# Kernel optimization log

Measured on AMD Instinct MI355X. Metric: run time of the kernel, lower is better.

## Reference

```python
import jax, jax.numpy as jnp
import numpy as np

N_HEADS = 8
D_MODEL = 256
HEAD_DEPTH = D_MODEL // N_HEADS
B, S = 2, 4096


def setup_inputs() -> dict:
    key = jax.random.key(0)
    ks = jax.random.split(key, 8)
    scale = 1.0 / np.sqrt(D_MODEL)
    return {
        "q": jax.random.normal(ks[0], (B, S, D_MODEL), dtype=jnp.float32),
        "k": jax.random.normal(ks[1], (B, S, D_MODEL), dtype=jnp.float32),
        "v": jax.random.normal(ks[2], (B, S, D_MODEL), dtype=jnp.float32),
        "mask": jax.random.randint(ks[3], (B, S, S), 0, 2).astype(jnp.bool_),
        "wq": jax.random.normal(ks[4], (D_MODEL, D_MODEL), dtype=jnp.float32) * scale,
        "wk": jax.random.normal(ks[5], (D_MODEL, D_MODEL), dtype=jnp.float32) * scale,
        "wv": jax.random.normal(ks[6], (D_MODEL, D_MODEL), dtype=jnp.float32) * scale,
        "w_out": jax.random.normal(ks[7], (D_MODEL, D_MODEL), dtype=jnp.float32) * scale,
    }


def _split_heads(x):
    # [B, S, D] -> [B, H, S, Dh]
    b, s, _ = x.shape
    return x.reshape(b, s, N_HEADS, HEAD_DEPTH).transpose(0, 2, 1, 3)


def reference(q, k, v, mask, wq, wk, wv, w_out):
    Q = _split_heads(q @ wq)
    K = _split_heads(k @ wk)
    V = _split_heads(v @ wv)
    # [B, H, Sq, Sk]
    scores = jnp.einsum('bhqd,bhkd->bhqk', Q, K) / jnp.sqrt(
        jnp.asarray(HEAD_DEPTH, dtype=Q.dtype))
    # mask True -> -inf, broadcast over heads
    scores = jnp.where(mask[:, None, :, :], -jnp.inf, scores)
    probs = jax.nn.softmax(scores, axis=-1)
    attn = jnp.einsum('bhqk,bhkd->bhqd', probs, V)
    attn = attn.transpose(0, 2, 1, 3).reshape(q.shape[0], -1, D_MODEL)
    return attn @ w_out
```

## Files before the change

### kernel.cpp

```cpp
#include <hip/hip_runtime.h>
#include <stdint.h>

typedef __bf16 bf16;
typedef __bf16 bf16x2 __attribute__((ext_vector_type(2)));
typedef __bf16 bf16x4 __attribute__((ext_vector_type(4)));
typedef __bf16 bf16x8 __attribute__((ext_vector_type(8)));
typedef float  f32x4  __attribute__((ext_vector_type(4)));
typedef float  f32x16 __attribute__((ext_vector_type(16)));
typedef float  float4v __attribute__((ext_vector_type(4)));
typedef int    int4v   __attribute__((ext_vector_type(4)));
typedef unsigned int uint;
typedef uint   uint4v  __attribute__((ext_vector_type(4)));
typedef unsigned long long ull;

#define QSCALE 0.25505003984214403f


__global__ __launch_bounds__(256) void transpose_w(
    const float* __restrict__ w0, const float* __restrict__ w1,
    const float* __restrict__ w2, const float* __restrict__ w3,
    bf16* __restrict__ WT) {
  const int wsel = blockIdx.z;
  const float* W = wsel == 0 ? w0 : wsel == 1 ? w1 : wsel == 2 ? w2 : w3;
  const int k0 = blockIdx.x * 64, n0 = blockIdx.y * 64;
  __shared__ __align__(16) bf16 t[64][72];
  const int tid = threadIdx.x;
  {
    const int kk = (tid >> 4) << 2;
    const int nn = (tid & 15) << 2;
#pragma unroll
    for (int r = 0; r < 4; ++r) {
      float4v a = *(const float4v*)(W + (size_t)(k0 + kk + r) * 256 + n0 + nn);
#pragma unroll
      for (int j = 0; j < 4; ++j) t[nn + j][kk + r] = (bf16)a[j];
    }
  }
  __syncthreads();
  {
    const int ni = tid >> 2;
    const int c  = (tid & 3) * 16;
    bf16x8 o0 = *(const bf16x8*)(&t[ni][c]);
    bf16x8 o1 = *(const bf16x8*)(&t[ni][c + 8]);
    bf16* dst = WT + (size_t)wsel * 65536 + (size_t)(n0 + ni) * 256 + k0 + c;
    *(bf16x8*)dst = o0;
    *(bf16x8*)(dst + 8) = o1;
  }
}

__global__ __launch_bounds__(256) void proj_pack(
    const float* __restrict__ xq, const float* __restrict__ xk, const float* __restrict__ xv,
    const bf16* __restrict__ WT,
    bf16* __restrict__ Qp, bf16* __restrict__ Kp, bf16* __restrict__ Vp,
    const int* __restrict__ mask, uint* __restrict__ M2) {
  __shared__ __align__(16) unsigned char smem[18432];
  const int tid = threadIdx.x;

  if (blockIdx.x < 1024) {
    uint* trans = (uint*)smem;
    const int pid = blockIdx.x;
    const int bb = pid >> 9;
    const int qt = (pid >> 2) & 127;
    const int kc = pid & 3;
    const int q0 = qt * 32;
    const int w = tid >> 6, l = tid & 63;
    const int d2 = l & 7;
    const int sh = 8 * d2;
    for (int batch = 0; batch < 4; ++batch) {
      int4v m[8];
#pragma unroll
      for (int u = 0; u < 8; ++u) {
        const int q_l = w * 8 + batch * 2 + (u >> 2);
        const int c = u & 3;
        m[u] = *(const int4v*)(mask + ((size_t)(bb * 4096 + q0 + q_l)) * 4096 +
                               kc * 1024 + c * 256 + 4 * l);
      }
#pragma unroll
      for (int u = 0; u < 8; ++u) {
        const int q_l = w * 8 + batch * 2 + (u >> 2);
        const int c = u & 3;
        uint out = 0;
#pragma unroll
        for (int i = 0; i < 4; ++i) {
          ull b = __ballot(m[u][i] != 0);
          out |= ((uint)(b >> sh) & 0xFFu) << (8 * i);
        }
        if (l < 8) trans[(c * 8 + d2) * 36 + q_l] = out;
      }
    }
    __syncthreads();
    {
      const int r = tid >> 3, c4 = (tid & 7) * 4;
      int4v a = *(const int4v*)(trans + r * 36 + c4);
      *(int4v*)(M2 + ((size_t)(bb * 128 + kc * 32 + r)) * 4096 + q0 + c4) = a;
    }
    return;
  }

  const int pb = blockIdx.x - 1024;
  const int z = pb >> 8;
  const int r8 = pb & 255;
  const int m0 = (r8 >> 1) * 64, n0 = (r8 & 1) * 128;
  const float* X = z == 0 ? xq : (z == 1 ? xk : xv);
  const bf16* wt = WT + (size_t)z * 65536;
  const int wave = tid >> 6, lane = tid & 63;
  const int nl = lane & 15, quad = lane >> 4;
  const int arow = m0 + wave * 16 + nl;
  const float* xrow = X + (size_t)arow * 256;

  f32x4 zero4 = {0.f, 0.f, 0.f, 0.f};
  f32x4 acc[8];
#pragma unroll
  for (int i = 0; i < 8; ++i) acc[i] = zero4;

  for (int ks = 0; ks < 8; ++ks) {
    float4v a0 = *(const float4v*)(xrow + ks * 32 + quad * 8);
    float4v a1 = *(const float4v*)(xrow + ks * 32 + quad * 8 + 4);
    bf16x8 af;
#pragma unroll
    for (int i = 0; i < 4; ++i) { af[i] = (bf16)a0[i]; af[4 + i] = (bf16)a1[i]; }
#pragma unroll
    for (int nf = 0; nf < 8; ++nf) {
      bf16x8 bfr = *(const bf16x8*)(wt + (size_t)(n0 + nf * 16 + nl) * 256 + ks * 32 + quad * 8);
      acc[nf] = __builtin_amdgcn_mfma_f32_16x16x32_bf16(af, bfr, acc[nf], 0, 0, 0);
    }
  }

  const int bq = m0 >> 12;
  const int s0 = m0 & 4095;
  const int posl = wave * 16 + quad * 4;

  if (z == 2) {
    bf16* tv = (bf16*)smem;
#pragma unroll
    for (int nf = 0; nf < 8; ++nf) {
      const int col = nf * 16 + nl;
      bf16x4 o;
#pragma unroll
      for (int rr = 0; rr < 4; ++rr) o[rr] = (bf16)acc[nf][rr];
      *(bf16x4*)(tv + (size_t)col * 72 + posl) = o;
    }
    __syncthreads();
    const int h2 = tid >> 6, ln = tid & 63;
    const int d = ln & 31, shalf = ln >> 5;
    const int h = (n0 >> 5) + h2;
    bf16* vb = Vp + (size_t)(bq * 8 + h) * 131072 + (size_t)(s0 >> 5) * 1024 + d * 8;
#pragma unroll
    for (int it = 0; it < 4; ++it) {
      const int blk = it >> 1, sub = (it & 1) * 2 + shalf;
      const int K0 = (sub >> 1) * 16 + (sub & 1) * 4;
      const bf16* src = tv + (size_t)(h2 * 32 + d) * 72 + blk * 32 + K0;
      bf16x4 g0 = *(const bf16x4*)(src);
      bf16x4 g1 = *(const bf16x4*)(src + 8);
      bf16x8 o;
#pragma unroll
      for (int j = 0; j < 4; ++j) { o[j] = g0[j]; o[4 + j] = g1[j]; }
      *(bf16x8*)(vb + (size_t)blk * 1024 + sub * 256) = o;
    }
  } else {
    bf16* tq = (bf16*)smem;
    const float scale = (z == 0) ? QSCALE : 1.0f;
#pragma unroll
    for (int nf = 0; nf < 8; ++nf) {
      const int col = nf * 16 + nl;
#pragma unroll
      for (int rr = 0; rr < 4; ++rr)
        tq[(size_t)(posl + rr) * 136 + col] = (bf16)(acc[nf][rr] * scale);
    }
    __syncthreads();
    bf16* Out = z == 0 ? Qp : Kp;
    const int h2 = tid >> 6, ln = tid & 63;
    const int h = (n0 >> 5) + h2;
    const int s = s0 + ln;
    bf16* ob = Out + (size_t)(bq * 8 + h) * 131072 + (size_t)(s >> 5) * 1024 + (s & 31) * 8;
#pragma unroll
    for (int sub = 0; sub < 4; ++sub) {
      bf16x8 o = *(const bf16x8*)(tq + (size_t)ln * 136 + h2 * 32 + sub * 8);
      *(bf16x8*)(ob + sub * 256) = o;
    }
  }
}

__global__ __launch_bounds__(128, 3) void attn_kernel(
    const bf16* __restrict__ Qp, const bf16* __restrict__ Kp,
    const bf16* __restrict__ Vp, const uint* __restrict__ M2,
    bf16* __restrict__ Og) {
  const int id = blockIdx.x;
  const int xcd = id & 7, slot = id >> 3;
  const int bh = xcd * 2 + (slot >> 6);
  const int qt = slot & 63;
  const int b = bh >> 3, h = bh & 7;
  const int tid = threadIdx.x, w = tid >> 6, lane = tid & 63;
  const int nl = lane & 31, half = lane >> 5;

  __shared__ __align__(16) bf16 T[64][40];

  const size_t bhbase = (size_t)bh * 131072;
  const int so0 = half * 256 + nl * 8;
  const int so1 = 512 + half * 256 + nl * 8;
  const int qg = qt * 64 + w * 32;

  const bf16* qb = Qp + bhbase + (size_t)(qg >> 5) * 1024;
  const bf16x8 qf0 = *(const bf16x8*)(qb + so0);
  const bf16x8 qf1 = *(const bf16x8*)(qb + so1);

  const bf16* Kb = Kp + bhbase;
  const bf16* Vb = Vp + bhbase;
  const uint* Mb = M2 + (size_t)b * 524288 + qg + nl;

  f32x16 z16;
#pragma unroll
  for (int i = 0; i < 16; ++i) z16[i] = 0.f;
  f32x16 acc = z16, lacc = z16;
  bf16x8 ones;
#pragma unroll
  for (int i = 0; i < 8; ++i) ones[i] = (bf16)1.0f;

  struct Frag { bf16x8 ka0, ka1, va0, va1; uint m; };
  auto LOADF = [&](int kdw) -> Frag {
    Frag f;
    const bf16* kc = Kb + (size_t)kdw * 1024;
    const bf16* vc = Vb + (size_t)kdw * 1024;
    f.ka0 = *(const bf16x8*)(kc + so0);
    f.ka1 = *(const bf16x8*)(kc + so1);
    f.va0 = *(const bf16x8*)(vc + so0);
    f.va1 = *(const bf16x8*)(vc + so1);
    f.m = Mb[(size_t)kdw * 4096];
    return f;
  };

  auto STEP = [&](const Frag& f) {
    const int minv = (int)((~f.m) >> half);
    f32x16 st = __builtin_amdgcn_mfma_f32_32x32x16_bf16(f.ka0, qf0, z16, 0, 0, 0);
    st = __builtin_amdgcn_mfma_f32_32x32x16_bf16(f.ka1, qf1, st, 0, 0, 0);

    uint pk[8];
#pragma unroll
    for (int g = 0; g < 4; ++g)
#pragma unroll
      for (int rp = 0; rp < 2; ++rp) {
        const int i = g * 4 + rp * 2;
        float e0 = __builtin_amdgcn_exp2f(st[i]);
        float e1 = __builtin_amdgcn_exp2f(st[i + 1]);
        const uint k0m = (uint)__builtin_amdgcn_sbfe(minv, 8 * (2 * rp) + 2 * g, 1);
        const uint k1m = (uint)__builtin_amdgcn_sbfe(minv, 8 * (2 * rp + 1) + 2 * g, 1);
        const uint u0 = __float_as_uint(e0) & k0m;
        const uint u1 = __float_as_uint(e1) & k1m;
        pk[g * 2 + rp] = __builtin_amdgcn_perm(u1, u0, 0x07060302u);
      }
    uint4v a0 = {pk[0], pk[1], pk[2], pk[3]};
    uint4v a1 = {pk[4], pk[5], pk[6], pk[7]};
    const bf16x8 pb0 = __builtin_bit_cast(bf16x8, a0);
    const bf16x8 pb1 = __builtin_bit_cast(bf16x8, a1);

    acc  = __builtin_amdgcn_mfma_f32_32x32x16_bf16(f.va0, pb0, acc, 0, 0, 0);
    lacc = __builtin_amdgcn_mfma_f32_32x32x16_bf16(ones,  pb0, lacc, 0, 0, 0);
    acc  = __builtin_amdgcn_mfma_f32_32x32x16_bf16(f.va1, pb1, acc, 0, 0, 0);
    lacc = __builtin_amdgcn_mfma_f32_32x32x16_bf16(ones,  pb1, lacc, 0, 0, 0);
  };

  Frag fa = LOADF(0), fb;
  for (int kdw = 0; kdw < 128; kdw += 2) {
    fb = LOADF(kdw + 1);
    STEP(fa);
    if (kdw + 2 < 128) fa = LOADF(kdw + 2);
    STEP(fb);
  }

  const float rl = 1.0f / lacc[0];
#pragma unroll
  for (int g = 0; g < 4; ++g)
#pragma unroll
    for (int rp = 0; rp < 2; ++rp) {
      const int i = g * 4 + rp * 2;
      const int d = rp * 2 + 8 * g + 4 * half;
      bf16x2 o;
      o[0] = (bf16)(acc[i] * rl);
      o[1] = (bf16)(acc[i + 1] * rl);
      *(bf16x2*)(&T[w * 32 + nl][d]) = o;
    }
  __syncthreads();
  {
    const int ql = tid & 63, rep = tid >> 6;
    bf16* obase = Og + ((size_t)(b * 4096 + qt * 64 + ql)) * 256 + h * 32;
#pragma unroll
    for (int c = 0; c < 2; ++c) {
      const int chunk = rep * 2 + c;
      bf16x8 o = *(const bf16x8*)(&T[ql][chunk * 8]);
      *(bf16x8*)(obase + chunk * 8) = o;
    }
  }
}

__global__ __launch_bounds__(256) void gemm_out(
    const bf16* __restrict__ A, const bf16* __restrict__ WTo, float* __restrict__ C) {
  const int m0 = blockIdx.x * 64, n0 = blockIdx.y * 64;
  const int tid = threadIdx.x, wave = tid >> 6, lane = tid & 63;
  const int nl = lane & 15, quad = lane >> 4;
  const int arow = m0 + wave * 16 + nl;

  f32x4 zero4 = {0.f, 0.f, 0.f, 0.f};
  f32x4 acc[4];
#pragma unroll
  for (int i = 0; i < 4; ++i) acc[i] = zero4;

  for (int ks = 0; ks < 8; ++ks) {
    bf16x8 af = *(const bf16x8*)(A + (size_t)arow * 256 + ks * 32 + quad * 8);
#pragma unroll
    for (int nf = 0; nf < 4; ++nf) {
      bf16x8 bfr = *(const bf16x8*)(WTo + (size_t)(n0 + nf * 16 + nl) * 256 + ks * 32 + quad * 8);
      acc[nf] = __builtin_amdgcn_mfma_f32_16x16x32_bf16(af, bfr, acc[nf], 0, 0, 0);
    }
  }
  const int Rbase = m0 + wave * 16 + quad * 4;
#pragma unroll
  for (int nf = 0; nf < 4; ++nf)
#pragma unroll
    for (int r = 0; r < 4; ++r)
      C[(size_t)(Rbase + r) * 256 + n0 + nf * 16 + nl] = acc[nf][r];
}

extern "C" void kernel_launch(void* const* d_in, const int* in_sizes, int n_in,
                              void* d_out, int out_size, void* d_ws, size_t ws_size,
                              hipStream_t stream) {
  const float* q  = (const float*)d_in[0];
  const float* k  = (const float*)d_in[1];
  const float* v  = (const float*)d_in[2];
  const int*  mask = (const int*)d_in[3];
  const float* wq = (const float*)d_in[4];
  const float* wk = (const float*)d_in[5];
  const float* wv = (const float*)d_in[6];
  const float* wo = (const float*)d_in[7];
  float* out = (float*)d_out;

  uint8_t* ws = (uint8_t*)d_ws;
  bf16* WT = (bf16*)ws;
  bf16* Qp = (bf16*)(ws + (512u << 10));
  bf16* Kp = Qp + 2097152;
  bf16* Vp = Kp + 2097152;
  uint* Mb = (uint*)((uint8_t*)(Vp + 2097152));
  bf16* Ao = (bf16*)((uint8_t*)Mb + (4u << 20));

  transpose_w<<<dim3(4, 4, 4), 256, 0, stream>>>(wq, wk, wv, wo, WT);
  proj_pack<<<dim3(1024 + 768), 256, 0, stream>>>(q, k, v, WT, Qp, Kp, Vp, mask, Mb);
  attn_kernel<<<dim3(1024), 128, 0, stream>>>(Qp, Kp, Vp, Mb, Ao);
  gemm_out<<<dim3(128, 4), 256, 0, stream>>>(Ao, WT + 3 * 65536, out);
}
```

Before: 333.9 us.

## Split attention key range across waves with shared-memory reduction of partial outputs

The attention kernel now gives each block one 32-query tile and splits the 4096 keys across four waves. Each wave accumulates partial numerators and row sums, which are then reduced in shared memory before normalization. Grid size doubles and block size goes to 256 threads, so more waves run per head-tile and each wave has a shorter serial loop, at the cost of extra shared-memory traffic and a reduction step. Separately, the mask-packing loop loads 16 mask vectors per batch instead of 8, putting more loads in flight.

```diff
diff --git a/kernel.cpp b/kernel.cpp
--- a/kernel.cpp
+++ b/kernel.cpp
@@ -65,18 +65,18 @@
     const int w = tid >> 6, l = tid & 63;
     const int d2 = l & 7;
     const int sh = 8 * d2;
-    for (int batch = 0; batch < 4; ++batch) {
-      int4v m[8];
-#pragma unroll
-      for (int u = 0; u < 8; ++u) {
-        const int q_l = w * 8 + batch * 2 + (u >> 2);
+    for (int batch = 0; batch < 2; ++batch) {
+      int4v m[16];
+#pragma unroll
+      for (int u = 0; u < 16; ++u) {
+        const int q_l = w * 8 + batch * 4 + (u >> 2);
         const int c = u & 3;
         m[u] = *(const int4v*)(mask + ((size_t)(bb * 4096 + q0 + q_l)) * 4096 +
                                kc * 1024 + c * 256 + 4 * l);
       }
 #pragma unroll
-      for (int u = 0; u < 8; ++u) {
-        const int q_l = w * 8 + batch * 2 + (u >> 2);
+      for (int u = 0; u < 16; ++u) {
+        const int q_l = w * 8 + batch * 4 + (u >> 2);
         const int c = u & 3;
         uint out = 0;
 #pragma unroll
@@ -180,26 +180,27 @@
   }
 }
 
-__global__ __launch_bounds__(128, 3) void attn_kernel(
+__global__ __launch_bounds__(256, 5) void attn_kernel(
     const bf16* __restrict__ Qp, const bf16* __restrict__ Kp,
     const bf16* __restrict__ Vp, const uint* __restrict__ M2,
     bf16* __restrict__ Og) {
   const int id = blockIdx.x;
   const int xcd = id & 7, slot = id >> 3;
-  const int bh = xcd * 2 + (slot >> 6);
-  const int qt = slot & 63;
+  const int bh = xcd * 2 + (slot >> 7);
+  const int qt = slot & 127;
   const int b = bh >> 3, h = bh & 7;
   const int tid = threadIdx.x, w = tid >> 6, lane = tid & 63;
   const int nl = lane & 31, half = lane >> 5;
 
-  __shared__ __align__(16) bf16 T[64][40];
+  __shared__ __align__(16) float Ored[4][32][36];
+  __shared__ float Lsum[4][32];
 
   const size_t bhbase = (size_t)bh * 131072;
   const int so0 = half * 256 + nl * 8;
   const int so1 = 512 + half * 256 + nl * 8;
-  const int qg = qt * 64 + w * 32;
-
-  const bf16* qb = Qp + bhbase + (size_t)(qg >> 5) * 1024;
+  const int qg = qt * 32;
+
+  const bf16* qb = Qp + bhbase + (size_t)qt * 1024;
   const bf16x8 qf0 = *(const bf16x8*)(qb + so0);
   const bf16x8 qf1 = *(const bf16x8*)(qb + so1);
 
@@ -258,36 +259,34 @@
     lacc = __builtin_amdgcn_mfma_f32_32x32x16_bf16(ones,  pb1, lacc, 0, 0, 0);
   };
 
-  Frag fa = LOADF(0), fb;
-  for (int kdw = 0; kdw < 128; kdw += 2) {
-    fb = LOADF(kdw + 1);
+  const int kbase = w * 32;
+  Frag fa = LOADF(kbase), fb;
+  for (int i = 0; i < 32; i += 2) {
+    fb = LOADF(kbase + i + 1);
     STEP(fa);
-    if (kdw + 2 < 128) fa = LOADF(kdw + 2);
+    if (i + 2 < 32) fa = LOADF(kbase + i + 2);
     STEP(fb);
   }
 
-  const float rl = 1.0f / lacc[0];
-#pragma unroll
-  for (int g = 0; g < 4; ++g)
-#pragma unroll
-    for (int rp = 0; rp < 2; ++rp) {
-      const int i = g * 4 + rp * 2;
-      const int d = rp * 2 + 8 * g + 4 * half;
-      bf16x2 o;
-      o[0] = (bf16)(acc[i] * rl);
-      o[1] = (bf16)(acc[i + 1] * rl);
-      *(bf16x2*)(&T[w * 32 + nl][d]) = o;
-    }
+#pragma unroll
+  for (int g = 0; g < 4; ++g) {
+    f32x4 v = {acc[g * 4], acc[g * 4 + 1], acc[g * 4 + 2], acc[g * 4 + 3]};
+    *(f32x4*)(&Ored[w][nl][8 * g + 4 * half]) = v;
+  }
+  if (half == 0) Lsum[w][nl] = lacc[0];
   __syncthreads();
   {
-    const int ql = tid & 63, rep = tid >> 6;
-    bf16* obase = Og + ((size_t)(b * 4096 + qt * 64 + ql)) * 256 + h * 32;
-#pragma unroll
-    for (int c = 0; c < 2; ++c) {
-      const int chunk = rep * 2 + c;
-      bf16x8 o = *(const bf16x8*)(&T[ql][chunk * 8]);
-      *(bf16x8*)(obase + chunk * 8) = o;
-    }
+    const int q = tid >> 3, dc = (tid & 7) * 4;
+    f32x4 s = *(const f32x4*)(&Ored[0][q][dc]);
+    f32x4 s1 = *(const f32x4*)(&Ored[1][q][dc]);
+    f32x4 s2 = *(const f32x4*)(&Ored[2][q][dc]);
+    f32x4 s3 = *(const f32x4*)(&Ored[3][q][dc]);
+    s += s1; s2 += s3; s += s2;
+    const float rl = 1.0f / (Lsum[0][q] + Lsum[1][q] + Lsum[2][q] + Lsum[3][q]);
+    bf16x4 o;
+#pragma unroll
+    for (int r = 0; r < 4; ++r) o[r] = (bf16)(s[r] * rl);
+    *(bf16x4*)(Og + ((size_t)(b * 4096 + qg + q)) * 256 + h * 32 + dc) = o;
   }
 }
 
@@ -342,6 +341,6 @@
 
   transpose_w<<<dim3(4, 4, 4), 256, 0, stream>>>(wq, wk, wv, wo, WT);
   proj_pack<<<dim3(1024 + 768), 256, 0, stream>>>(q, k, v, WT, Qp, Kp, Vp, mask, Mb);
-  attn_kernel<<<dim3(1024), 128, 0, stream>>>(Qp, Kp, Vp, Mb, Ao);
+  attn_kernel<<<dim3(2048), 256, 0, stream>>>(Qp, Kp, Vp, Mb, Ao);
   gemm_out<<<dim3(128, 4), 256, 0, stream>>>(Ao, WT + 3 * 65536, out);
 }
```

Result: no change. 331.0 us (-0.9%).
